# Kernel tuning notes

Hardware: AMD Instinct MI355X
Metric: run time of the kernel (lower is better)

The kernel has to match this reference:

```python
import jax, jax.numpy as jnp
import numpy as np
from math import sqrt

B, N, D = 16, 4096, 128
M = 64 * 24  # mem_size_per_joint * num_joints


def setup_inputs() -> dict:
    key = jax.random.key(0)
    kx, km = jax.random.split(key)
    x = jax.random.normal(kx, (B, N, D), dtype=jnp.float32)
    mem = jax.random.normal(km, (1, D, M), dtype=jnp.float32)  # N(0,1) init as in torch
    return {"x": x, "mem": mem}


def reference(x, mem):
    # x: (B, N, D); mem: (1, D, M)
    d = x.shape[-1]
    w = mem[0]  # (D, M)
    # logits = bmm(m_key (B,M,D), x_ (B,D,N)) / sqrt(D)  -> (B, M, N)
    logits = jnp.einsum('dm,bnd->bmn', w, x) / sqrt(d)
    # softmax over the memory axis (dim=1 in torch layout)
    attn = jax.nn.softmax(logits, axis=1)  # (B, M, N)
    # x_new = bmm(m (B,D,M), attn) -> (B,D,N); output permuted to (B,N,D)
    out = jnp.einsum('dm,bmn->bnd', w, attn)
    return out
```

## Files before the change

kernel.cpp:

```cpp
#include <hip/hip_runtime.h>
#include <math.h>


#define Bdim 16
#define Ndim 4096
#define Ddim 128
#define Mdim 1536
#define NT 64
#define NTHREADS 256
#define NSESS 12
#define NFRAG 24576

typedef __attribute__((ext_vector_type(8)))  _Float16 f16x8;
typedef __attribute__((ext_vector_type(4)))  _Float16 f16x4;
typedef __attribute__((ext_vector_type(16))) float    f32x16;

__global__ void jamb_prep(const float* __restrict__ w,
                          _Float16* __restrict__ wt,
                          _Float16* __restrict__ wd) {
    const int tid = blockIdx.x * 256 + threadIdx.x;
    const float SC = 0.08838834764831843f;
    if (tid < NFRAG) {
        const int f    = tid;
        const int l    = f & 63;
        const int fs   = f >> 6;
        const int ks   = fs & 7;
        const int mt   = fs >> 3;
        const int m    = mt * 32 + (l & 31);
        const int d0   = ks * 16 + (l >> 5) * 8;
        f16x8 pk;
        #pragma unroll
        for (int j = 0; j < 8; ++j)
            pk[j] = (_Float16)(w[(size_t)(d0 + j) * Mdim + m] * SC);
        *(f16x8*)&wt[(size_t)f * 8] = pk;
    } else {
        const int f    = tid - NFRAG;
        const int l    = f & 63;
        const int fs   = f >> 6;
        const int km   = fs % 96;
        const int dt   = fs / 96;
        const int d    = dt * 32 + (l & 31);
        const int m0   = km * 16 + (l >> 5) * 8;
        const float* src = w + (size_t)d * Mdim + m0;
        const float4 v0 = *(const float4*)src;
        const float4 v1 = *(const float4*)(src + 4);
        f16x8 pk;
        pk[0] = (_Float16)v0.x; pk[1] = (_Float16)v0.y;
        pk[2] = (_Float16)v0.z; pk[3] = (_Float16)v0.w;
        pk[4] = (_Float16)v1.x; pk[5] = (_Float16)v1.y;
        pk[6] = (_Float16)v1.z; pk[7] = (_Float16)v1.w;
        *(f16x8*)&wd[(size_t)f * 8] = pk;
    }
}

__global__ __launch_bounds__(NTHREADS, 4)
void jamb_mfma_kernel(const float* __restrict__ x,
                      const _Float16* __restrict__ wt,
                      const _Float16* __restrict__ wd,
                      float* __restrict__ out) {
    __shared__ __align__(16) _Float16 xs[NT * 128];
    __shared__ __align__(16) _Float16 Pbuf[NT * 128];
    __shared__ float redsum[4][NT];

    const int t    = threadIdx.x;
    const int w    = t >> 6;
    const int l    = t & 63;
    const int c32  = l & 31;
    const int half = l >> 5;

    const int blk   = blockIdx.x;
    const int b     = blk >> 6;
    const int nbase = (blk & 63) * NT;

    {
        const float* xb = x + (size_t)(b * Ndim + nbase) * Ddim;
        #pragma unroll
        for (int i = 0; i < 8; ++i) {
            const int f   = t + i * 256;
            const int row = f >> 5;
            const int c4  = (f & 31) * 4;
            const float4 v = *(const float4*)(xb + row * Ddim + c4);
            f16x4 pk;
            pk[0] = (_Float16)v.x; pk[1] = (_Float16)v.y;
            pk[2] = (_Float16)v.z; pk[3] = (_Float16)v.w;
            const int g = ((c4 >> 3) ^ (row & 15)) << 3;
            *(f16x4*)&xs[row * 128 + g + (c4 & 7)] = pk;
        }
    }
    __syncthreads();

    const f16x8* WT = (const f16x8*)wt;
    const f16x8* WD = (const f16x8*)wd;

    float sums[2] = {0.f, 0.f};
    f32x16 c0 = {0.f}, c1 = {0.f};
    #pragma unroll
    for (int r = 0; r < 16; ++r) { c0[r] = 0.f; c1[r] = 0.f; }

    const int swz = c32 & 15;

    #pragma unroll 1
    for (int q = 0; q < NSESS; ++q) {
        f32x16 a0 = {0.f}, a1 = {0.f};
        #pragma unroll
        for (int r = 0; r < 16; ++r) { a0[r] = 0.f; a1[r] = 0.f; }
        #pragma unroll
        for (int ks = 0; ks < 8; ++ks) {
            const f16x8 af = WT[((q * 4 + w) * 8 + ks) * 64 + l];
            const int g = (((ks * 2 + half) ^ swz) << 3);
            const f16x8 b0 = *(const f16x8*)&xs[c32 * 128 + g];
            const f16x8 b1 = *(const f16x8*)&xs[(32 + c32) * 128 + g];
            a0 = __builtin_amdgcn_mfma_f32_32x32x16_f16(af, b0, a0, 0, 0, 0);
            a1 = __builtin_amdgcn_mfma_f32_32x32x16_f16(af, b1, a1, 0, 0, 0);
        }

        #pragma unroll
        for (int rq = 0; rq < 4; ++rq) {
            const int gq = ((w * 4 + rq) ^ swz) << 3;
            const int oq = half * 4;
            {
                const float e0 = __expf(a0[rq * 4 + 0]);
                const float e1 = __expf(a0[rq * 4 + 1]);
                const float e2 = __expf(a0[rq * 4 + 2]);
                const float e3 = __expf(a0[rq * 4 + 3]);
                sums[0] += (e0 + e1) + (e2 + e3);
                f16x4 pk;
                pk[0] = (_Float16)e0; pk[1] = (_Float16)e1;
                pk[2] = (_Float16)e2; pk[3] = (_Float16)e3;
                *(f16x4*)&Pbuf[c32 * 128 + gq + oq] = pk;
            }
            {
                const float e0 = __expf(a1[rq * 4 + 0]);
                const float e1 = __expf(a1[rq * 4 + 1]);
                const float e2 = __expf(a1[rq * 4 + 2]);
                const float e3 = __expf(a1[rq * 4 + 3]);
                sums[1] += (e0 + e1) + (e2 + e3);
                f16x4 pk;
                pk[0] = (_Float16)e0; pk[1] = (_Float16)e1;
                pk[2] = (_Float16)e2; pk[3] = (_Float16)e3;
                *(f16x4*)&Pbuf[(32 + c32) * 128 + gq + oq] = pk;
            }
        }
        __syncthreads();

        #pragma unroll
        for (int km = 0; km < 8; ++km) {
            const f16x8 wdf = WD[(w * 96 + q * 8 + km) * 64 + l];
            const int g = (((km * 2 + half) ^ swz) << 3);
            const f16x8 p0 = *(const f16x8*)&Pbuf[c32 * 128 + g];
            const f16x8 p1 = *(const f16x8*)&Pbuf[(32 + c32) * 128 + g];
            c0 = __builtin_amdgcn_mfma_f32_32x32x16_f16(wdf, p0, c0, 0, 0, 0);
            c1 = __builtin_amdgcn_mfma_f32_32x32x16_f16(wdf, p1, c1, 0, 0, 0);
        }
        __syncthreads();
    }

    sums[0] += __shfl_xor(sums[0], 32, 64);
    sums[1] += __shfl_xor(sums[1], 32, 64);
    if (half == 0) {
        redsum[w][c32]      = sums[0];
        redsum[w][32 + c32] = sums[1];
    }
    __syncthreads();

    const float inv0 = 1.f / (redsum[0][c32] + redsum[1][c32] +
                              redsum[2][c32] + redsum[3][c32]);
    const float inv1 = 1.f / (redsum[0][32 + c32] + redsum[1][32 + c32] +
                              redsum[2][32 + c32] + redsum[3][32 + c32]);

    #pragma unroll
    for (int rq = 0; rq < 4; ++rq) {
        const int d = w * 32 + rq * 8 + half * 4;
        {
            float* op = out + (size_t)(b * Ndim + nbase + c32) * Ddim + d;
            float4 o;
            o.x = c0[rq * 4 + 0] * inv0; o.y = c0[rq * 4 + 1] * inv0;
            o.z = c0[rq * 4 + 2] * inv0; o.w = c0[rq * 4 + 3] * inv0;
            *(float4*)op = o;
        }
        {
            float* op = out + (size_t)(b * Ndim + nbase + 32 + c32) * Ddim + d;
            float4 o;
            o.x = c1[rq * 4 + 0] * inv1; o.y = c1[rq * 4 + 1] * inv1;
            o.z = c1[rq * 4 + 2] * inv1; o.w = c1[rq * 4 + 3] * inv1;
            *(float4*)op = o;
        }
    }
}

extern "C" void kernel_launch(void* const* d_in, const int* in_sizes, int n_in,
                              void* d_out, int out_size, void* d_ws, size_t ws_size,
                              hipStream_t stream) {
    const float* x = (const float*)d_in[0];
    const float* w = (const float*)d_in[1];
    float* out = (float*)d_out;
    (void)in_sizes; (void)n_in; (void)out_size; (void)ws_size;

    _Float16* wt = (_Float16*)d_ws;
    _Float16* wd = wt + Ddim * Mdim;

    jamb_prep<<<dim3((2 * NFRAG) / 256), dim3(256), 0, stream>>>(w, wt, wd);
    jamb_mfma_kernel<<<dim3((Bdim * Ndim) / NT), dim3(NTHREADS), 0, stream>>>(x, wt, wd, out);
}
```

Measured before the change: 140.3 us.

## Keep softmax probabilities in registers and split M across waves with final reduction

Each wave now owns a slice of the memory axis and keeps its exponentiated logits in registers. They are rearranged with cross-half lane shuffles directly into MFMA B-operand layout, and the value-side weights are pre-permuted in the prep kernel to match. This removes the per-iteration LDS round-trip for probabilities and both __syncthreads in the main loop. In exchange, each wave holds 8 output accumulators (all 128 D for 64 rows), which raises register pressure, so occupancy drops to 2 blocks per SM. A four-way cross-wave reduction through shared memory is added at the end.

```diff
diff --git a/kernel.cpp b/kernel.cpp
--- a/kernel.cpp
+++ b/kernel.cpp
@@ -8,11 +8,12 @@
 #define Mdim 1536
 #define NT 64
 #define NTHREADS 256
-#define NSESS 12
+#define NMT 12
 #define NFRAG 24576
 
 typedef __attribute__((ext_vector_type(8)))  _Float16 f16x8;
 typedef __attribute__((ext_vector_type(4)))  _Float16 f16x4;
+typedef __attribute__((ext_vector_type(2)))  __fp16   fp16x2;
 typedef __attribute__((ext_vector_type(16))) float    f32x16;
 
 __global__ void jamb_prep(const float* __restrict__ w,
@@ -40,33 +41,32 @@
         const int km   = fs % 96;
         const int dt   = fs / 96;
         const int d    = dt * 32 + (l & 31);
-        const int m0   = km * 16 + (l >> 5) * 8;
-        const float* src = w + (size_t)d * Mdim + m0;
-        const float4 v0 = *(const float4*)src;
-        const float4 v1 = *(const float4*)(src + 4);
+        const int h8   = (l >> 5) * 8;
         f16x8 pk;
-        pk[0] = (_Float16)v0.x; pk[1] = (_Float16)v0.y;
-        pk[2] = (_Float16)v0.z; pk[3] = (_Float16)v0.w;
-        pk[4] = (_Float16)v1.x; pk[5] = (_Float16)v1.y;
-        pk[6] = (_Float16)v1.z; pk[7] = (_Float16)v1.w;
+        #pragma unroll
+        for (int j = 0; j < 8; ++j) {
+            const int k  = h8 + j;
+            const int ms = k < 8 ? k : (k < 12 ? k + 4 : k - 4);
+            pk[j] = (_Float16)(w[(size_t)d * Mdim + km * 16 + ms]);
+        }
         *(f16x8*)&wd[(size_t)f * 8] = pk;
     }
 }
 
-__global__ __launch_bounds__(NTHREADS, 4)
+__global__ __launch_bounds__(NTHREADS, 2)
 void jamb_mfma_kernel(const float* __restrict__ x,
                       const _Float16* __restrict__ wt,
                       const _Float16* __restrict__ wd,
                       float* __restrict__ out) {
-    __shared__ __align__(16) _Float16 xs[NT * 128];
-    __shared__ __align__(16) _Float16 Pbuf[NT * 128];
+    __shared__ __align__(16) float sbuf[4 * 32 * 64];
     __shared__ float redsum[4][NT];
-
-    const int t    = threadIdx.x;
-    const int w    = t >> 6;
-    const int l    = t & 63;
-    const int c32  = l & 31;
-    const int half = l >> 5;
+    _Float16* xs = (_Float16*)sbuf;
+
+    const int t   = threadIdx.x;
+    const int w   = t >> 6;
+    const int l   = t & 63;
+    const int c32 = l & 31;
+    const int h   = l >> 5;
 
     const int blk   = blockIdx.x;
     const int b     = blk >> 6;
@@ -93,98 +93,116 @@
     const f16x8* WD = (const f16x8*)wd;
 
     float sums[2] = {0.f, 0.f};
-    f32x16 c0 = {0.f}, c1 = {0.f};
+    f32x16 c[2][4];
     #pragma unroll
-    for (int r = 0; r < 16; ++r) { c0[r] = 0.f; c1[r] = 0.f; }
+    for (int nt = 0; nt < 2; ++nt)
+        #pragma unroll
+        for (int dt = 0; dt < 4; ++dt)
+            #pragma unroll
+            for (int r = 0; r < 16; ++r) c[nt][dt][r] = 0.f;
 
     const int swz = c32 & 15;
 
     #pragma unroll 1
-    for (int q = 0; q < NSESS; ++q) {
-        f32x16 a0 = {0.f}, a1 = {0.f};
-        #pragma unroll
-        for (int r = 0; r < 16; ++r) { a0[r] = 0.f; a1[r] = 0.f; }
+    for (int i = 0; i < NMT; ++i) {
+        const int mt = i * 4 + w;
+
+        f32x16 a[2];
+        #pragma unroll
+        for (int nt = 0; nt < 2; ++nt)
+            #pragma unroll
+            for (int r = 0; r < 16; ++r) a[nt][r] = 0.f;
         #pragma unroll
         for (int ks = 0; ks < 8; ++ks) {
-            const f16x8 af = WT[((q * 4 + w) * 8 + ks) * 64 + l];
-            const int g = (((ks * 2 + half) ^ swz) << 3);
+            const f16x8 af = WT[((mt * 8 + ks) * 64) + l];
+            const int g = (((ks * 2 + h) ^ swz) << 3);
             const f16x8 b0 = *(const f16x8*)&xs[c32 * 128 + g];
             const f16x8 b1 = *(const f16x8*)&xs[(32 + c32) * 128 + g];
-            a0 = __builtin_amdgcn_mfma_f32_32x32x16_f16(af, b0, a0, 0, 0, 0);
-            a1 = __builtin_amdgcn_mfma_f32_32x32x16_f16(af, b1, a1, 0, 0, 0);
-        }
-
-        #pragma unroll
-        for (int rq = 0; rq < 4; ++rq) {
-            const int gq = ((w * 4 + rq) ^ swz) << 3;
-            const int oq = half * 4;
-            {
-                const float e0 = __expf(a0[rq * 4 + 0]);
-                const float e1 = __expf(a0[rq * 4 + 1]);
-                const float e2 = __expf(a0[rq * 4 + 2]);
-                const float e3 = __expf(a0[rq * 4 + 3]);
-                sums[0] += (e0 + e1) + (e2 + e3);
-                f16x4 pk;
-                pk[0] = (_Float16)e0; pk[1] = (_Float16)e1;
-                pk[2] = (_Float16)e2; pk[3] = (_Float16)e3;
-                *(f16x4*)&Pbuf[c32 * 128 + gq + oq] = pk;
-            }
-            {
-                const float e0 = __expf(a1[rq * 4 + 0]);
-                const float e1 = __expf(a1[rq * 4 + 1]);
-                const float e2 = __expf(a1[rq * 4 + 2]);
-                const float e3 = __expf(a1[rq * 4 + 3]);
-                sums[1] += (e0 + e1) + (e2 + e3);
-                f16x4 pk;
-                pk[0] = (_Float16)e0; pk[1] = (_Float16)e1;
-                pk[2] = (_Float16)e2; pk[3] = (_Float16)e3;
-                *(f16x4*)&Pbuf[(32 + c32) * 128 + gq + oq] = pk;
-            }
-        }
-        __syncthreads();
-
-        #pragma unroll
-        for (int km = 0; km < 8; ++km) {
-            const f16x8 wdf = WD[(w * 96 + q * 8 + km) * 64 + l];
-            const int g = (((km * 2 + half) ^ swz) << 3);
-            const f16x8 p0 = *(const f16x8*)&Pbuf[c32 * 128 + g];
-            const f16x8 p1 = *(const f16x8*)&Pbuf[(32 + c32) * 128 + g];
-            c0 = __builtin_amdgcn_mfma_f32_32x32x16_f16(wdf, p0, c0, 0, 0, 0);
-            c1 = __builtin_amdgcn_mfma_f32_32x32x16_f16(wdf, p1, c1, 0, 0, 0);
-        }
-        __syncthreads();
+            a[0] = __builtin_amdgcn_mfma_f32_32x32x16_f16(af, b0, a[0], 0, 0, 0);
+            a[1] = __builtin_amdgcn_mfma_f32_32x32x16_f16(af, b1, a[1], 0, 0, 0);
+        }
+
+        unsigned pk[2][8];
+        #pragma unroll
+        for (int nt = 0; nt < 2; ++nt) {
+            #pragma unroll
+            for (int p = 0; p < 8; ++p) {
+                const float e0 = __expf(a[nt][2 * p]);
+                const float e1 = __expf(a[nt][2 * p + 1]);
+                sums[nt] += e0 + e1;
+                union { fp16x2 hh; unsigned u; } cv;
+                cv.hh = __builtin_amdgcn_cvt_pkrtz(e0, e1);
+                pk[nt][p] = cv.u;
+            }
+        }
+
+        f16x8 pf[2][2];
+        #pragma unroll
+        for (int nt = 0; nt < 2; ++nt) {
+            #pragma unroll
+            for (int g = 0; g < 2; ++g) {
+                const int bse = g * 4;
+                const unsigned o0 = h ? pk[nt][bse + 2] : pk[nt][bse + 0];
+                const unsigned o1 = h ? pk[nt][bse + 3] : pk[nt][bse + 1];
+                const unsigned s0 = h ? pk[nt][bse + 0] : pk[nt][bse + 2];
+                const unsigned s1 = h ? pk[nt][bse + 1] : pk[nt][bse + 3];
+                const unsigned r0 = __shfl_xor(s0, 32, 64);
+                const unsigned r1 = __shfl_xor(s1, 32, 64);
+                union { unsigned u[4]; f16x8 v; } cv;
+                cv.u[0] = o0; cv.u[1] = o1; cv.u[2] = r0; cv.u[3] = r1;
+                pf[nt][g] = cv.v;
+            }
+        }
+
+        #pragma unroll
+        for (int dt = 0; dt < 4; ++dt) {
+            #pragma unroll
+            for (int g = 0; g < 2; ++g) {
+                const f16x8 wdf = WD[((dt * 96 + mt * 2 + g) * 64) + l];
+                c[0][dt] = __builtin_amdgcn_mfma_f32_32x32x16_f16(wdf, pf[0][g], c[0][dt], 0, 0, 0);
+                c[1][dt] = __builtin_amdgcn_mfma_f32_32x32x16_f16(wdf, pf[1][g], c[1][dt], 0, 0, 0);
+            }
+        }
     }
 
     sums[0] += __shfl_xor(sums[0], 32, 64);
     sums[1] += __shfl_xor(sums[1], 32, 64);
-    if (half == 0) {
+    if (h == 0) {
         redsum[w][c32]      = sums[0];
         redsum[w][32 + c32] = sums[1];
     }
     __syncthreads();
 
-    const float inv0 = 1.f / (redsum[0][c32] + redsum[1][c32] +
-                              redsum[2][c32] + redsum[3][c32]);
-    const float inv1 = 1.f / (redsum[0][32 + c32] + redsum[1][32 + c32] +
-                              redsum[2][32 + c32] + redsum[3][32 + c32]);
+    const int en  = t >> 2;
+    const int ed0 = (t & 3) * 8;
+    const float invn = 1.f / (redsum[0][en] + redsum[1][en] +
+                              redsum[2][en] + redsum[3][en]);
 
     #pragma unroll
-    for (int rq = 0; rq < 4; ++rq) {
-        const int d = w * 32 + rq * 8 + half * 4;
-        {
-            float* op = out + (size_t)(b * Ndim + nbase + c32) * Ddim + d;
-            float4 o;
-            o.x = c0[rq * 4 + 0] * inv0; o.y = c0[rq * 4 + 1] * inv0;
-            o.z = c0[rq * 4 + 2] * inv0; o.w = c0[rq * 4 + 3] * inv0;
-            *(float4*)op = o;
-        }
-        {
-            float* op = out + (size_t)(b * Ndim + nbase + 32 + c32) * Ddim + d;
-            float4 o;
-            o.x = c1[rq * 4 + 0] * inv1; o.y = c1[rq * 4 + 1] * inv1;
-            o.z = c1[rq * 4 + 2] * inv1; o.w = c1[rq * 4 + 3] * inv1;
-            *(float4*)op = o;
-        }
+    for (int dt = 0; dt < 4; ++dt) {
+        #pragma unroll
+        for (int nt = 0; nt < 2; ++nt) {
+            #pragma unroll
+            for (int r = 0; r < 16; ++r) {
+                const int row = (r & 3) + 8 * (r >> 2) + 4 * h;
+                sbuf[(w * 32 + row) * 64 + nt * 32 + c32] = c[nt][dt][r];
+            }
+        }
+        __syncthreads();
+        float o[8];
+        #pragma unroll
+        for (int k = 0; k < 8; ++k) {
+            o[k] = (sbuf[(0 * 32 + ed0 + k) * 64 + en] +
+                    sbuf[(1 * 32 + ed0 + k) * 64 + en] +
+                    sbuf[(2 * 32 + ed0 + k) * 64 + en] +
+                    sbuf[(3 * 32 + ed0 + k) * 64 + en]) * invn;
+        }
+        float* op = out + (size_t)(b * Ndim + nbase + en) * Ddim + dt * 32 + ed0;
+        float4 v0; v0.x = o[0]; v0.y = o[1]; v0.z = o[2]; v0.w = o[3];
+        float4 v1; v1.x = o[4]; v1.y = o[5]; v1.z = o[6]; v1.w = o[7];
+        *(float4*)op = v0;
+        *(float4*)(op + 4) = v1;
+        __syncthreads();
     }
 }
 
```

Result: slower. 197.6 us (+40.8%).
